# Kernel tuning notes

Hardware: AMD Instinct MI355X
Metric: run time of the kernel (lower is better)

Reference implementation:

```python
import jax, jax.numpy as jnp
import numpy as np
import math

B, C, W, H = 4, 96, 64, 64
MID, OUT = 24, 256
EPS = 1e-5


def setup_inputs() -> dict:
    key = jax.random.key(0)
    ks = jax.random.split(key, 8)
    s = lambda *sh: 1.0 / math.sqrt(sh[-1])
    return {
        "rgb": jax.random.normal(ks[0], (B, C, W, H), dtype=jnp.float32),
        "dep": jax.random.normal(ks[1], (B, C, W, H), dtype=jnp.float32),
        "Wd": jax.random.normal(ks[2], (C, C), dtype=jnp.float32) * s(C, C),   # dept 1x1 conv
        "Wr": jax.random.normal(ks[3], (C, C), dtype=jnp.float32) * s(C, C),   # rgb 1x1 conv
        "Wm1": jax.random.normal(ks[4], (MID, C), dtype=jnp.float32) * s(MID, C),
        "bn1_g": jnp.ones((MID,), dtype=jnp.float32),
        "bn1_b": jnp.zeros((MID,), dtype=jnp.float32),
        "Wm2": jax.random.normal(ks[5], (OUT, MID), dtype=jnp.float32) * s(OUT, MID),
        "bn2_g": jnp.ones((OUT,), dtype=jnp.float32),
        "bn2_b": jnp.zeros((OUT,), dtype=jnp.float32),
    }


def _bn_relu(x, gamma, beta):
    # training-mode BatchNorm over batch dim (spatial is 1x1), biased variance, then ReLU
    mu = x.mean(axis=0)
    var = x.var(axis=0)
    y = (x - mu) * jax.lax.rsqrt(var + EPS) * gamma + beta
    return jax.nn.relu(y)


def reference(rgb, dep, Wd, Wr, Wm1, bn1_g, bn1_b, Wm2, bn2_g, bn2_b):
    b, c, w, h = rgb.shape
    hw = w * h
    rgbd = rgb + dep
    # 1x1 convs as channel matmuls -> [B, C, HW]
    pr = jnp.einsum('oc,bchw->bohw', Wr, rgb).reshape(b, c, hw)
    pd = jnp.einsum('oc,bchw->bohw', Wd, dep).reshape(b, c, hw)
    # energy[b, n, m] = proj_rgb^T proj_dep / sqrt(C)   -> [B, HW, HW]
    energy = jnp.einsum('bcn,bcm->bnm', pr, pd) / math.sqrt(c)
    # torch Softmax(dim=1) on [B, HW, HW] normalizes over the first HW axis
    att = jax.nn.softmax(energy, axis=1)
    att_r = jnp.einsum('bcn,bnm->bcm', pr, att)
    att_b = jnp.einsum('bcn,bnm->bcm', pd, att)
    out = (att_r + att_b).reshape(b, c, w, h) + rgbd
    gap = out.mean(axis=(2, 3))  # [B, C] (AdaptiveAvgPool2d(1) squeezed)
    h1 = _bn_relu(gap @ Wm1.T, bn1_g, bn1_b)        # [B, 24]
    gate = _bn_relu(h1 @ Wm2.T, bn2_g, bn2_b)       # [B, OUT] (ReLU, as in source)
    return gate[:, :, None, None]                    # [B, OUT, 1, 1]
```

## Files before the change

kernel.cpp:

```cpp
#include <hip/hip_runtime.h>

#define HW 4096
#define NC 96
#define NB 4
#define MID 24
#define NOUT 256
#define BEPS 1e-5f
#define SCALE_E 0.10206207261596575f

typedef unsigned short u16;
typedef short bf16x8 __attribute__((ext_vector_type(8)));
typedef unsigned short u16x8 __attribute__((ext_vector_type(8)));
typedef float f32x16 __attribute__((ext_vector_type(16)));

__device__ __forceinline__ u16 bfh(float x) {
  unsigned u = __float_as_uint(x);
  return (u16)((u + 0x7FFFu + ((u >> 16) & 1u)) >> 16);
}
__device__ __forceinline__ float bf2f(u16 h) {
  return __uint_as_float(((unsigned)h) << 16);
}

__launch_bounds__(256)
__global__ void k_prep(const float* __restrict__ rgb, const float* __restrict__ dep,
                       const float* __restrict__ Wr, const float* __restrict__ Wd,
                       float* __restrict__ psum, u16* __restrict__ prF, u16* __restrict__ pdF) {
  __shared__ u16 buf[2][128][48];
  const int tid = threadIdx.x;
  const int slot = tid & 63;
  const int og = __builtin_amdgcn_readfirstlane(tid >> 6);
  const int b = blockIdx.y, q = blockIdx.z;
  const int n0 = blockIdx.x * 128;
  const int obase = q * 24 + og * 6;

  float ar[6][2], ad[6][2];
  #pragma unroll
  for (int o = 0; o < 6; ++o) { ar[o][0] = ar[o][1] = ad[o][0] = ad[o][1] = 0.f; }

  const float* rb = rgb + (size_t)b * NC * HW + n0;
  const float* db = dep + (size_t)b * NC * HW + n0;
  #pragma unroll 4
  for (int c = 0; c < NC; ++c) {
    float2 xr = ((const float2*)(rb + (size_t)c * HW))[slot];
    float2 xd = ((const float2*)(db + (size_t)c * HW))[slot];
    #pragma unroll
    for (int o = 0; o < 6; ++o) {
      float wr = Wr[(obase + o) * NC + c];
      float wd = Wd[(obase + o) * NC + c];
      ar[o][0] = fmaf(wr, xr.x, ar[o][0]);
      ar[o][1] = fmaf(wr, xr.y, ar[o][1]);
      ad[o][0] = fmaf(wd, xd.x, ad[o][0]);
      ad[o][1] = fmaf(wd, xd.y, ad[o][1]);
    }
  }

  #pragma unroll
  for (int o = 0; o < 6; ++o) {
    float2 ps = make_float2(ar[o][0] + ad[o][0], ar[o][1] + ad[o][1]);
    *(float2*)&psum[((size_t)b * NC + obase + o) * HW + n0 + slot * 2] = ps;
    #pragma unroll
    for (int j = 0; j < 2; ++j) {
      int nl = slot * 2 + j;
      int ol = og * 6 + o;
      u16 h = bfh(ar[o][j]);
      buf[0][nl][ol] = h;
      buf[0][nl][24 + ol] = bfh(ar[o][j] - bf2f(h));
      u16 h2 = bfh(ad[o][j]);
      buf[1][nl][ol] = h2;
      buf[1][nl][24 + ol] = bfh(ad[o][j] - bf2f(h2));
    }
  }
  __syncthreads();

  for (int idx = tid; idx < 1536; idx += 256) {
    int arr = idx / 768;
    int rem = idx % 768;
    int piece = rem >> 7;
    int nl = rem & 127;
    int hl = piece >= 3 ? 1 : 0;
    int p = piece - hl * 3;
    int c8 = q * 3 + p;
    int ks = c8 >> 1, khalf = c8 & 1;
    int tile = (n0 >> 5) + (nl >> 5);
    u16* dst = (arr ? pdF : prF) + (size_t)b * HW * 192
             + ((tile * 12 + ks * 2 + hl) << 9) + ((khalf * 32 + (nl & 31)) << 3);
    *(u16x8*)dst = *(const u16x8*)&buf[arr][nl][hl * 24 + p * 8];
  }
}

template <int PASS>
__launch_bounds__(256, 2)
__global__ void k_energy(const u16* __restrict__ At, const u16* __restrict__ Bt,
                         const float* __restrict__ nlz, float* __restrict__ part) {
  __shared__ float red[2][128];
  const int tid = threadIdx.x;
  const int lane = tid & 63, wid = tid >> 6;
  const int wA = wid >> 1, wB = wid & 1;
  const int b = blockIdx.z;
  const int flat = blockIdx.y * 32 + blockIdx.x;
  const int by = (flat & 7) * 4 + ((flat >> 3) & 3);
  const int bx = flat >> 5;
  const int a0 = by * 128;
  const int c0 = bx * 128;
  const u16* Ab = At + (size_t)b * HW * 192;
  const u16* Bb = Bt + (size_t)b * HW * 192;
  const int tA0 = by * 4 + wA * 2;
  const int tB0 = bx * 4 + wB * 2;

  bf16x8 Ah[2][6], Al[2][6];
  #pragma unroll
  for (int ta = 0; ta < 2; ++ta)
    #pragma unroll
    for (int ks = 0; ks < 6; ++ks) {
      const u16* pa = Ab + (((tA0 + ta) * 12 + ks * 2) << 9) + (lane << 3);
      Ah[ta][ks] = *(const bf16x8*)pa;
      Al[ta][ks] = *(const bf16x8*)(pa + 512);
    }

  f32x16 acc[2][2];
  #pragma unroll
  for (int ta = 0; ta < 2; ++ta)
    #pragma unroll
    for (int tb = 0; tb < 2; ++tb)
      #pragma unroll
      for (int q = 0; q < 16; ++q) acc[ta][tb][q] = 0.f;

  #pragma unroll
  for (int ks = 0; ks < 6; ++ks) {
    #pragma unroll
    for (int tb = 0; tb < 2; ++tb) {
      const u16* pb = Bb + (((tB0 + tb) * 12 + ks * 2) << 9) + (lane << 3);
      bf16x8 bh = *(const bf16x8*)pb;
      #pragma unroll
      for (int ta = 0; ta < 2; ++ta) {
        acc[ta][tb] = __builtin_amdgcn_mfma_f32_32x32x16_bf16(Ah[ta][ks], bh, acc[ta][tb], 0, 0, 0);
        acc[ta][tb] = __builtin_amdgcn_mfma_f32_32x32x16_bf16(Al[ta][ks], bh, acc[ta][tb], 0, 0, 0);
      }
    }
  }

  float csum[2] = {0.f, 0.f};
  float nlzv = 0.f;
  if (PASS) nlzv = nlz[(size_t)b * HW + a0 + wA * 64 + lane];
  #pragma unroll
  for (int ta = 0; ta < 2; ++ta) {
    #pragma unroll
    for (int q = 0; q < 16; ++q) {
      float bias = 0.f;
      if (PASS) {
        int src = ta * 32 + (q & 3) + 8 * (q >> 2) + 4 * (lane >> 5);
        bias = __shfl(nlzv, src, 64);
      }
      #pragma unroll
      for (int tb = 0; tb < 2; ++tb)
        csum[tb] += __expf(fmaf(acc[ta][tb][q], SCALE_E, bias));
    }
  }
  #pragma unroll
  for (int tb = 0; tb < 2; ++tb) csum[tb] += __shfl_xor(csum[tb], 32, 64);
  if (lane < 32) {
    #pragma unroll
    for (int tb = 0; tb < 2; ++tb) red[wA][wB * 64 + tb * 32 + lane] = csum[tb];
  }
  __syncthreads();
  if (tid < 128)
    part[((size_t)by * NB + b) * HW + c0 + tid] = red[0][tid] + red[1][tid];
}

__global__ void k_zred(const float* __restrict__ zpart, float* __restrict__ nlz) {
  int idx = blockIdx.x * 256 + threadIdx.x;
  float s = 0.f;
  #pragma unroll
  for (int t = 0; t < 32; ++t) s += zpart[(size_t)t * (NB * HW) + idx];
  nlz[idx] = -logf(s);
}

__global__ void k_sred(const float* __restrict__ spart, float* __restrict__ sv) {
  int idx = blockIdx.x * 256 + threadIdx.x;
  float a = 0.f;
  #pragma unroll
  for (int t = 0; t < 32; ++t) a += spart[(size_t)t * (NB * HW) + idx];
  sv[idx] = a;
}

__launch_bounds__(256)
__global__ void k_gap(const float* __restrict__ psum, const float* __restrict__ rgb,
                      const float* __restrict__ dep, const float* __restrict__ sv,
                      float* __restrict__ gap) {
  const int c = blockIdx.x, b = blockIdx.y;
  const size_t off = ((size_t)b * NC + c) * HW;
  const float* pp = psum + off;
  const float* rp = rgb + off;
  const float* dp = dep + off;
  const float* sp = sv + (size_t)b * HW;
  float a1 = 0.f, a2 = 0.f;
  for (int n = threadIdx.x * 4; n < HW; n += 1024) {
    float4 p = *(const float4*)&pp[n];
    float4 s4 = *(const float4*)&sp[n];
    float4 r4 = *(const float4*)&rp[n];
    float4 d4 = *(const float4*)&dp[n];
    a1 += p.x * s4.x + p.y * s4.y + p.z * s4.z + p.w * s4.w;
    a2 += (r4.x + d4.x) + (r4.y + d4.y) + (r4.z + d4.z) + (r4.w + d4.w);
  }
  #pragma unroll
  for (int o = 32; o > 0; o >>= 1) {
    a1 += __shfl_down(a1, o, 64);
    a2 += __shfl_down(a2, o, 64);
  }
  __shared__ float r1[4], r2[4];
  const int wv = threadIdx.x >> 6;
  if ((threadIdx.x & 63) == 0) { r1[wv] = a1; r2[wv] = a2; }
  __syncthreads();
  if (threadIdx.x == 0) {
    float t1 = r1[0] + r1[1] + r1[2] + r1[3];
    float t2 = r2[0] + r2[1] + r2[2] + r2[3];
    gap[b * NC + c] = (t1 + t2) * (1.0f / HW);
  }
}

__launch_bounds__(256)
__global__ void k_mlp(const float* __restrict__ gap,
                      const float* __restrict__ Wm1, const float* __restrict__ g1,
                      const float* __restrict__ b1,
                      const float* __restrict__ Wm2, const float* __restrict__ g2,
                      const float* __restrict__ b2, float* __restrict__ out) {
  __shared__ float gl[NB * NC];
  __shared__ float h[NB * MID];
  __shared__ float h1r[NB * MID];
  __shared__ float h2[NB * NOUT];
  const int tid = threadIdx.x;
  for (int i = tid; i < NB * NC; i += 256) gl[i] = gap[i];
  __syncthreads();

  if (tid < NB * MID) {
    int b = tid / MID, j = tid % MID;
    float acc = 0.f;
    #pragma unroll
    for (int c = 0; c < NC; ++c) acc += gl[b * NC + c] * Wm1[j * NC + c];
    h[b * MID + j] = acc;
  }
  __syncthreads();

  if (tid < MID) {
    float x0 = h[0 * MID + tid], x1 = h[1 * MID + tid];
    float x2 = h[2 * MID + tid], x3 = h[3 * MID + tid];
    float mu = 0.25f * (x0 + x1 + x2 + x3);
    float d0 = x0 - mu, d1 = x1 - mu, d2 = x2 - mu, d3 = x3 - mu;
    float v = 0.25f * (d0 * d0 + d1 * d1 + d2 * d2 + d3 * d3);
    float sc = g1[tid] * rsqrtf(v + BEPS);
    float bb = b1[tid];
    h1r[0 * MID + tid] = fmaxf(d0 * sc + bb, 0.f);
    h1r[1 * MID + tid] = fmaxf(d1 * sc + bb, 0.f);
    h1r[2 * MID + tid] = fmaxf(d2 * sc + bb, 0.f);
    h1r[3 * MID + tid] = fmaxf(d3 * sc + bb, 0.f);
  }
  __syncthreads();

  for (int idx = tid; idx < NB * NOUT; idx += 256) {
    int b = idx >> 8, o = idx & 255;
    float acc = 0.f;
    #pragma unroll
    for (int j = 0; j < MID; ++j) acc += h1r[b * MID + j] * Wm2[o * MID + j];
    h2[b * NOUT + o] = acc;
  }
  __syncthreads();

  if (tid < NOUT) {
    float x0 = h2[0 * NOUT + tid], x1 = h2[1 * NOUT + tid];
    float x2 = h2[2 * NOUT + tid], x3 = h2[3 * NOUT + tid];
    float mu = 0.25f * (x0 + x1 + x2 + x3);
    float d0 = x0 - mu, d1 = x1 - mu, d2 = x2 - mu, d3 = x3 - mu;
    float v = 0.25f * (d0 * d0 + d1 * d1 + d2 * d2 + d3 * d3);
    float sc = g2[tid] * rsqrtf(v + BEPS);
    float bb = b2[tid];
    out[0 * NOUT + tid] = fmaxf(d0 * sc + bb, 0.f);
    out[1 * NOUT + tid] = fmaxf(d1 * sc + bb, 0.f);
    out[2 * NOUT + tid] = fmaxf(d2 * sc + bb, 0.f);
    out[3 * NOUT + tid] = fmaxf(d3 * sc + bb, 0.f);
  }
}

extern "C" void kernel_launch(void* const* d_in, const int* in_sizes, int n_in,
                              void* d_out, int out_size, void* d_ws, size_t ws_size,
                              hipStream_t stream) {
  const float* rgb   = (const float*)d_in[0];
  const float* dep   = (const float*)d_in[1];
  const float* Wd    = (const float*)d_in[2];
  const float* Wr    = (const float*)d_in[3];
  const float* Wm1   = (const float*)d_in[4];
  const float* bn1_g = (const float*)d_in[5];
  const float* bn1_b = (const float*)d_in[6];
  const float* Wm2   = (const float*)d_in[7];
  const float* bn2_g = (const float*)d_in[8];
  const float* bn2_b = (const float*)d_in[9];
  float* out = (float*)d_out;

  char* w = (char*)d_ws;
  u16* prF = (u16*)w;             w += (size_t)NB * HW * 192 * 2;
  u16* pdF = (u16*)w;             w += (size_t)NB * HW * 192 * 2;
  float* psum  = (float*)w;       w += (size_t)NB * NC * HW * 4;
  float* zpart = (float*)w;       w += (size_t)32 * NB * HW * 4;
  float* nlz   = (float*)w;       w += (size_t)NB * HW * 4;
  float* spart = (float*)w;       w += (size_t)32 * NB * HW * 4;
  float* sv    = (float*)w;       w += (size_t)NB * HW * 4;
  float* gap   = (float*)w;       w += (size_t)NB * NC * 4;

  k_prep<<<dim3(HW / 128, NB, 4), 256, 0, stream>>>(rgb, dep, Wr, Wd, psum, prF, pdF);
  k_energy<0><<<dim3(32, 32, NB), 256, 0, stream>>>(prF, pdF, nullptr, zpart);
  k_zred<<<NB * HW / 256, 256, 0, stream>>>(zpart, nlz);
  k_energy<1><<<dim3(32, 32, NB), 256, 0, stream>>>(pdF, prF, nlz, spart);
  k_sred<<<NB * HW / 256, 256, 0, stream>>>(spart, sv);
  k_gap<<<dim3(NC, NB), 256, 0, stream>>>(psum, rgb, dep, sv, gap);
  k_mlp<<<1, 256, 0, stream>>>(gap, Wm1, bn1_g, bn1_b, Wm2, bn2_g, bn2_b, out);
}
```

Baseline: 99.81 us.

## Drop bf16 hi/lo split for energy GEMM, fuse z-reduction and rgbd sums

Stores the projections as a single bf16 term instead of a hi+lo pair, which halves both the MFMA count and the operand bytes in both energy passes. The k_zred kernel is removed, and the column-normalizer reduction plus log is folded into the start of the second energy pass. The rgb+dep channel sums are computed in k_prep via wave shuffles, so k_gap no longer re-reads rgb and dep. The trade-off is lower precision in the energy logits, which feed an exponent and could hurt accuracy. Each pass-1 block also re-reduces its 32 partials.

Result: slower. 112.1 us (+12.3%).

```diff
diff --git a/kernel.cpp b/kernel.cpp
--- a/kernel.cpp
+++ b/kernel.cpp
@@ -17,15 +17,14 @@
   unsigned u = __float_as_uint(x);
   return (u16)((u + 0x7FFFu + ((u >> 16) & 1u)) >> 16);
 }
-__device__ __forceinline__ float bf2f(u16 h) {
-  return __uint_as_float(((unsigned)h) << 16);
-}
 
 __launch_bounds__(256)
 __global__ void k_prep(const float* __restrict__ rgb, const float* __restrict__ dep,
                        const float* __restrict__ Wr, const float* __restrict__ Wd,
-                       float* __restrict__ psum, u16* __restrict__ prF, u16* __restrict__ pdF) {
-  __shared__ u16 buf[2][128][48];
+                       float* __restrict__ psum, u16* __restrict__ prF, u16* __restrict__ pdF,
+                       float* __restrict__ rsum_part) {
+  __shared__ u16 buf[2][128][24];
+  __shared__ float rsumL[NC];
   const int tid = threadIdx.x;
   const int slot = tid & 63;
   const int og = __builtin_amdgcn_readfirstlane(tid >> 6);
@@ -52,6 +51,16 @@
       ad[o][0] = fmaf(wd, xd.x, ad[o][0]);
       ad[o][1] = fmaf(wd, xd.y, ad[o][1]);
     }
+    if (og == 0) {
+      float t = (xr.x + xd.x) + (xr.y + xd.y);
+      t += __shfl_xor(t, 1, 64);
+      t += __shfl_xor(t, 2, 64);
+      t += __shfl_xor(t, 4, 64);
+      t += __shfl_xor(t, 8, 64);
+      t += __shfl_xor(t, 16, 64);
+      t += __shfl_xor(t, 32, 64);
+      if (slot == 0) rsumL[c] = t;
+    }
   }
 
   #pragma unroll
@@ -62,37 +71,34 @@
     for (int j = 0; j < 2; ++j) {
       int nl = slot * 2 + j;
       int ol = og * 6 + o;
-      u16 h = bfh(ar[o][j]);
-      buf[0][nl][ol] = h;
-      buf[0][nl][24 + ol] = bfh(ar[o][j] - bf2f(h));
-      u16 h2 = bfh(ad[o][j]);
-      buf[1][nl][ol] = h2;
-      buf[1][nl][24 + ol] = bfh(ad[o][j] - bf2f(h2));
-    }
-  }
-  __syncthreads();
-
-  for (int idx = tid; idx < 1536; idx += 256) {
-    int arr = idx / 768;
-    int rem = idx % 768;
+      buf[0][nl][ol] = bfh(ar[o][j]);
+      buf[1][nl][ol] = bfh(ad[o][j]);
+    }
+  }
+  __syncthreads();
+
+  for (int idx = tid; idx < 768; idx += 256) {
+    int arr = idx / 384;
+    int rem = idx % 384;
     int piece = rem >> 7;
     int nl = rem & 127;
-    int hl = piece >= 3 ? 1 : 0;
-    int p = piece - hl * 3;
-    int c8 = q * 3 + p;
+    int c8 = q * 3 + piece;
     int ks = c8 >> 1, khalf = c8 & 1;
     int tile = (n0 >> 5) + (nl >> 5);
-    u16* dst = (arr ? pdF : prF) + (size_t)b * HW * 192
-             + ((tile * 12 + ks * 2 + hl) << 9) + ((khalf * 32 + (nl & 31)) << 3);
-    *(u16x8*)dst = *(const u16x8*)&buf[arr][nl][hl * 24 + p * 8];
-  }
+    u16* dst = (arr ? pdF : prF) + (size_t)b * HW * 96
+             + ((tile * 6 + ks) << 9) + ((khalf * 32 + (nl & 31)) << 3);
+    *(u16x8*)dst = *(const u16x8*)&buf[arr][nl][piece * 8];
+  }
+  if (q == 0 && tid < NC)
+    rsum_part[((size_t)blockIdx.x * NB + b) * NC + tid] = rsumL[tid];
 }
 
 template <int PASS>
 __launch_bounds__(256, 2)
 __global__ void k_energy(const u16* __restrict__ At, const u16* __restrict__ Bt,
-                         const float* __restrict__ nlz, float* __restrict__ part) {
+                         const float* __restrict__ zin, float* __restrict__ part) {
   __shared__ float red[2][128];
+  __shared__ float nlzL[128];
   const int tid = threadIdx.x;
   const int lane = tid & 63, wid = tid >> 6;
   const int wA = wid >> 1, wB = wid & 1;
@@ -102,20 +108,27 @@
   const int bx = flat >> 5;
   const int a0 = by * 128;
   const int c0 = bx * 128;
-  const u16* Ab = At + (size_t)b * HW * 192;
-  const u16* Bb = Bt + (size_t)b * HW * 192;
+  const u16* Ab = At + (size_t)b * HW * 96;
+  const u16* Bb = Bt + (size_t)b * HW * 96;
   const int tA0 = by * 4 + wA * 2;
   const int tB0 = bx * 4 + wB * 2;
 
-  bf16x8 Ah[2][6], Al[2][6];
+  if (PASS) {
+    if (tid < 128) {
+      float s = 0.f;
+      #pragma unroll
+      for (int t = 0; t < 32; ++t) s += zin[((size_t)t * NB + b) * HW + a0 + tid];
+      nlzL[tid] = -__logf(s);
+    }
+    __syncthreads();
+  }
+
+  bf16x8 Ah[2][6];
   #pragma unroll
   for (int ta = 0; ta < 2; ++ta)
     #pragma unroll
-    for (int ks = 0; ks < 6; ++ks) {
-      const u16* pa = Ab + (((tA0 + ta) * 12 + ks * 2) << 9) + (lane << 3);
-      Ah[ta][ks] = *(const bf16x8*)pa;
-      Al[ta][ks] = *(const bf16x8*)(pa + 512);
-    }
+    for (int ks = 0; ks < 6; ++ks)
+      Ah[ta][ks] = *(const bf16x8*)(Ab + (((tA0 + ta) * 6 + ks) << 9) + (lane << 3));
 
   f32x16 acc[2][2];
   #pragma unroll
@@ -129,19 +142,16 @@
   for (int ks = 0; ks < 6; ++ks) {
     #pragma unroll
     for (int tb = 0; tb < 2; ++tb) {
-      const u16* pb = Bb + (((tB0 + tb) * 12 + ks * 2) << 9) + (lane << 3);
-      bf16x8 bh = *(const bf16x8*)pb;
+      bf16x8 bh = *(const bf16x8*)(Bb + (((tB0 + tb) * 6 + ks) << 9) + (lane << 3));
       #pragma unroll
-      for (int ta = 0; ta < 2; ++ta) {
+      for (int ta = 0; ta < 2; ++ta)
         acc[ta][tb] = __builtin_amdgcn_mfma_f32_32x32x16_bf16(Ah[ta][ks], bh, acc[ta][tb], 0, 0, 0);
-        acc[ta][tb] = __builtin_amdgcn_mfma_f32_32x32x16_bf16(Al[ta][ks], bh, acc[ta][tb], 0, 0, 0);
-      }
     }
   }
 
   float csum[2] = {0.f, 0.f};
   float nlzv = 0.f;
-  if (PASS) nlzv = nlz[(size_t)b * HW + a0 + wA * 64 + lane];
+  if (PASS) nlzv = nlzL[wA * 64 + lane];
   #pragma unroll
   for (int ta = 0; ta < 2; ++ta) {
     #pragma unroll
@@ -167,14 +177,6 @@
     part[((size_t)by * NB + b) * HW + c0 + tid] = red[0][tid] + red[1][tid];
 }
 
-__global__ void k_zred(const float* __restrict__ zpart, float* __restrict__ nlz) {
-  int idx = blockIdx.x * 256 + threadIdx.x;
-  float s = 0.f;
-  #pragma unroll
-  for (int t = 0; t < 32; ++t) s += zpart[(size_t)t * (NB * HW) + idx];
-  nlz[idx] = -logf(s);
-}
-
 __global__ void k_sred(const float* __restrict__ spart, float* __restrict__ sv) {
   int idx = blockIdx.x * 256 + threadIdx.x;
   float a = 0.f;
@@ -184,37 +186,29 @@
 }
 
 __launch_bounds__(256)
-__global__ void k_gap(const float* __restrict__ psum, const float* __restrict__ rgb,
-                      const float* __restrict__ dep, const float* __restrict__ sv,
-                      float* __restrict__ gap) {
+__global__ void k_gap(const float* __restrict__ psum, const float* __restrict__ rsum_part,
+                      const float* __restrict__ sv, float* __restrict__ gap) {
   const int c = blockIdx.x, b = blockIdx.y;
-  const size_t off = ((size_t)b * NC + c) * HW;
-  const float* pp = psum + off;
-  const float* rp = rgb + off;
-  const float* dp = dep + off;
+  const float* pp = psum + ((size_t)b * NC + c) * HW;
   const float* sp = sv + (size_t)b * HW;
-  float a1 = 0.f, a2 = 0.f;
+  float a1 = 0.f;
   for (int n = threadIdx.x * 4; n < HW; n += 1024) {
     float4 p = *(const float4*)&pp[n];
     float4 s4 = *(const float4*)&sp[n];
-    float4 r4 = *(const float4*)&rp[n];
-    float4 d4 = *(const float4*)&dp[n];
     a1 += p.x * s4.x + p.y * s4.y + p.z * s4.z + p.w * s4.w;
-    a2 += (r4.x + d4.x) + (r4.y + d4.y) + (r4.z + d4.z) + (r4.w + d4.w);
-  }
-  #pragma unroll
-  for (int o = 32; o > 0; o >>= 1) {
-    a1 += __shfl_down(a1, o, 64);
-    a2 += __shfl_down(a2, o, 64);
-  }
-  __shared__ float r1[4], r2[4];
+  }
+  #pragma unroll
+  for (int o = 32; o > 0; o >>= 1) a1 += __shfl_down(a1, o, 64);
+  __shared__ float r1[4];
   const int wv = threadIdx.x >> 6;
-  if ((threadIdx.x & 63) == 0) { r1[wv] = a1; r2[wv] = a2; }
+  if ((threadIdx.x & 63) == 0) r1[wv] = a1;
   __syncthreads();
   if (threadIdx.x == 0) {
     float t1 = r1[0] + r1[1] + r1[2] + r1[3];
-    float t2 = r2[0] + r2[1] + r2[2] + r2[3];
-    gap[b * NC + c] = (t1 + t2) * (1.0f / HW);
+    float a2 = 0.f;
+    #pragma unroll
+    for (int t = 0; t < 32; ++t) a2 += rsum_part[((size_t)t * NB + b) * NC + c];
+    gap[b * NC + c] = (t1 + a2) * (1.0f / HW);
   }
 }
 
@@ -296,20 +290,19 @@
   float* out = (float*)d_out;
 
   char* w = (char*)d_ws;
-  u16* prF = (u16*)w;             w += (size_t)NB * HW * 192 * 2;
-  u16* pdF = (u16*)w;             w += (size_t)NB * HW * 192 * 2;
+  u16* prF = (u16*)w;             w += (size_t)NB * HW * 96 * 2;
+  u16* pdF = (u16*)w;             w += (size_t)NB * HW * 96 * 2;
   float* psum  = (float*)w;       w += (size_t)NB * NC * HW * 4;
   float* zpart = (float*)w;       w += (size_t)32 * NB * HW * 4;
-  float* nlz   = (float*)w;       w += (size_t)NB * HW * 4;
   float* spart = (float*)w;       w += (size_t)32 * NB * HW * 4;
   float* sv    = (float*)w;       w += (size_t)NB * HW * 4;
+  float* rsum  = (float*)w;       w += (size_t)32 * NB * NC * 4;
   float* gap   = (float*)w;       w += (size_t)NB * NC * 4;
 
-  k_prep<<<dim3(HW / 128, NB, 4), 256, 0, stream>>>(rgb, dep, Wr, Wd, psum, prF, pdF);
+  k_prep<<<dim3(HW / 128, NB, 4), 256, 0, stream>>>(rgb, dep, Wr, Wd, psum, prF, pdF, rsum);
   k_energy<0><<<dim3(32, 32, NB), 256, 0, stream>>>(prF, pdF, nullptr, zpart);
-  k_zred<<<NB * HW / 256, 256, 0, stream>>>(zpart, nlz);
-  k_energy<1><<<dim3(32, 32, NB), 256, 0, stream>>>(pdF, prF, nlz, spart);
+  k_energy<1><<<dim3(32, 32, NB), 256, 0, stream>>>(pdF, prF, zpart, spart);
   k_sred<<<NB * HW / 256, 256, 0, stream>>>(spart, sv);
-  k_gap<<<dim3(NC, NB), 256, 0, stream>>>(psum, rgb, dep, sv, gap);
+  k_gap<<<dim3(NC, NB), 256, 0, stream>>>(psum, rsum, sv, gap);
   k_mlp<<<1, 256, 0, stream>>>(gap, Wm1, bn1_g, bn1_b, Wm2, bn2_g, bn2_b, out);
 }
```
